# Optimization experiments

Measured on AMD Instinct MI355X. Metric: run time of the kernel, lower is better.

The kernel has to match this reference:

```python
import jax, jax.numpy as jnp
import numpy as np

NUM_HEADS = 16
D_MODEL = 1024
ROPE_THETA = 10000.0


def rope_cos_sin(H, W, head_dim, theta):
    # SAM2/SAM3 axial RoPE: first half of complex dims encode x, second half y.
    n = H * W
    t = jnp.arange(n)
    tx = (t % W).astype(jnp.float32)
    ty = (t // W).astype(jnp.float32)
    # freqs: 1 / theta^(arange(0, dim, 4)[:dim//4] / dim)
    exps = jnp.arange(0, head_dim, 4)[: head_dim // 4].astype(jnp.float32) / head_dim
    freqs = 1.0 / (theta ** exps)  # (head_dim//4,)
    ang = jnp.concatenate([tx[:, None] * freqs, ty[:, None] * freqs], axis=-1)  # (N, head_dim//2)
    return jnp.cos(ang), jnp.sin(ang)


def apply_rope(x, cos, sin):
    # x: (B, nh, N, D); pairs of features treated as complex numbers
    B, nh, N, D = x.shape
    xr = x.reshape(B, nh, N, D // 2, 2)
    xe, xo = xr[..., 0], xr[..., 1]
    oe = xe * cos - xo * sin
    oo = xe * sin + xo * cos
    return jnp.stack([oe, oo], axis=-1).reshape(B, nh, N, D)


def setup_inputs() -> dict:
    key = jax.random.key(0)
    ks = jax.random.split(key, 12)
    C = D_MODEL
    s = 1.0 / np.sqrt(C)
    inp = {
        "q": jax.random.normal(ks[0], (2, 2048, C), dtype=jnp.float32),
        "k": jax.random.normal(ks[1], (2, 2112, C), dtype=jnp.float32),
        "v": jax.random.normal(ks[2], (2, 2112, C), dtype=jnp.float32),
        "Wq": jax.random.normal(ks[3], (C, C), dtype=jnp.float32) * s,
        "bq": jax.random.normal(ks[4], (C,), dtype=jnp.float32) * s,
        "Wk": jax.random.normal(ks[5], (C, C), dtype=jnp.float32) * s,
        "bk": jax.random.normal(ks[6], (C,), dtype=jnp.float32) * s,
        "Wv": jax.random.normal(ks[7], (C, C), dtype=jnp.float32) * s,
        "bv": jax.random.normal(ks[8], (C,), dtype=jnp.float32) * s,
        "Wo": jax.random.normal(ks[9], (C, C), dtype=jnp.float32) * s,
        "bo": jax.random.normal(ks[10], (C,), dtype=jnp.float32) * s,
        "q_h": 32,
        "q_w": 64,
        "num_final_k_to_exclude": 64,
    }
    return inp


def reference(q, k, v, Wq, bq, Wk, bk, Wv, bv, Wo, bo, q_h, q_w, num_final_k_to_exclude):
    B, Nq, C = q.shape
    Nk = k.shape[1]
    nh = NUM_HEADS
    d = C // nh
    # QKV projections -> (B, nh, N, d)
    qh = (q @ Wq + bq).reshape(B, Nq, nh, d).transpose(0, 2, 1, 3)
    kh = (k @ Wk + bk).reshape(B, Nk, nh, d).transpose(0, 2, 1, 3)
    vh = (v @ Wv + bv).reshape(B, Nk, nh, d).transpose(0, 2, 1, 3)
    # RoPE on q and on first num_k_keep keys (exclude trailing pointer tokens)
    n_keep = Nk - num_final_k_to_exclude  # == q_h * q_w == Nq here
    cos, sin = rope_cos_sin(q_h, q_w, d, ROPE_THETA)
    qh = apply_rope(qh, cos, sin)
    k_rot = apply_rope(kh[:, :, :n_keep], cos, sin)
    kh = jnp.concatenate([k_rot, kh[:, :, n_keep:]], axis=2)
    # scaled dot-product attention
    scale = 1.0 / np.sqrt(d)
    scores = jnp.einsum("bhqd,bhkd->bhqk", qh, kh) * scale
    probs = jax.nn.softmax(scores, axis=-1)
    attn = jnp.einsum("bhqk,bhkd->bhqd", probs, vh)
    out = attn.transpose(0, 2, 1, 3).reshape(B, Nq, C)
    return out @ Wo + bo
```

## Files before the change

### kernel.cpp

```cpp
#include <hip/hip_runtime.h>

#define B_ 2
#define NQ 2048
#define NK 2112
#define CD 1024
#define NH 16
#define HD 64

typedef unsigned short u16;
typedef unsigned int u32;
typedef __attribute__((ext_vector_type(8))) __bf16 bf16x8;
typedef __attribute__((ext_vector_type(4))) float f32x4;

#define GPTR(p) ((const __attribute__((address_space(1))) void*)(p))
#define LPTR(p) ((__attribute__((address_space(3))) void*)(p))
#define GLL16(g, l) __builtin_amdgcn_global_load_lds(GPTR(g), LPTR(l), 16, 0, 0)

__device__ __forceinline__ u16 f2bf(float f) {
  u32 u = __float_as_uint(f);
  u32 r = u + 0x7fffu + ((u >> 16) & 1u);
  return (u16)(r >> 16);
}
__device__ __forceinline__ float bf2f(u16 h) { return __uint_as_float(((u32)h) << 16); }

#define SC 0.18033688011112042f
#define NEGL2T 0.8304820237f
#define FSTEP 0.5623413252f

__global__ void prep_kernel(const float* __restrict__ q, const float* __restrict__ k,
                            const float* __restrict__ v, u16* __restrict__ qb,
                            u16* __restrict__ kb, u16* __restrict__ vb,
                            const float* __restrict__ W0, const float* __restrict__ W1,
                            const float* __restrict__ W2, const float* __restrict__ W3,
                            u16* __restrict__ T0, u16* __restrict__ T1,
                            u16* __restrict__ T2, u16* __restrict__ T3) {
  __shared__ u16 tile[32][33];
  int y = blockIdx.y;
  int t = threadIdx.x;
  if (y < 3) {
    const float* src = (y == 0) ? q : (y == 1) ? k : v;
    u16* dst = (y == 0) ? qb : (y == 1) ? kb : vb;
    int n4 = (y == 0) ? (B_ * NQ * CD / 4) : (B_ * NK * CD / 4);
    int i = blockIdx.x * 256 + t;
    if (i >= n4) return;
    float4 vv = ((const float4*)src)[i];
    ushort4 o;
    o.x = f2bf(vv.x); o.y = f2bf(vv.y); o.z = f2bf(vv.z); o.w = f2bf(vv.w);
    ((ushort4*)dst)[i] = o;
  } else {
    int x = blockIdx.x;
    if (x >= 4096) return;
    int which = x >> 10, xy = x & 1023;
    const float* src = (which == 0) ? W0 : (which == 1) ? W1 : (which == 2) ? W2 : W3;
    u16* dst = (which == 0) ? T0 : (which == 1) ? T1 : (which == 2) ? T2 : T3;
    int r0 = (xy >> 5) * 32, c0 = (xy & 31) * 32;
    int row = t >> 3, c4 = (t & 7) * 4;
    float4 vv = *(const float4*)&src[(r0 + row) * 1024 + c0 + c4];
    tile[row][c4 + 0] = f2bf(vv.x);
    tile[row][c4 + 1] = f2bf(vv.y);
    tile[row][c4 + 2] = f2bf(vv.z);
    tile[row][c4 + 3] = f2bf(vv.w);
    __syncthreads();
    ushort4 o;
    o.x = tile[c4 + 0][row];
    o.y = tile[c4 + 1][row];
    o.z = tile[c4 + 2][row];
    o.w = tile[c4 + 3][row];
    *(ushort4*)&dst[(c0 + row) * 1024 + r0 + c4] = o;
  }
}

__global__ __launch_bounds__(256, 2) void gemm_qkv(
    const u16* __restrict__ qb, const u16* __restrict__ kb, const u16* __restrict__ vb,
    const u16* __restrict__ wqt, const u16* __restrict__ wkt, const u16* __restrict__ wvt,
    const float* __restrict__ bq, const float* __restrict__ bk, const float* __restrict__ bv,
    u16* __restrict__ Qh, u16* __restrict__ Kh, u16* __restrict__ Vt) {
  __shared__ u16 As[128 * 32];
  __shared__ u16 Bs[128 * 32];
  const int z = blockIdx.z;
  if (z == 0 && blockIdx.y >= 32) return;
  const u16* A = (z == 0) ? qb : (z == 1) ? kb : vb;
  const u16* Bt = (z == 0) ? wqt : (z == 1) ? wkt : wvt;
  const float* bias = (z == 0) ? bq : (z == 1) ? bk : bv;
  const int BR = (z == 0) ? NQ : NK;

  const int t = threadIdx.x;
  const int lane = t & 63, w = t >> 6;
  const int lc = lane & 15, lq = lane >> 4;
  const int m0 = blockIdx.y * 128, n0 = blockIdx.x * 128;
  const int wm = (w >> 1) * 64, wn = (w & 1) * 64;
  f32x4 acc[4][4] = {};
  const u16* ga = A + (m0 + (t >> 2)) * 1024 + (t & 3) * 8;
  const u16* gb = Bt + (n0 + (t >> 2)) * 1024 + (t & 3) * 8;
  char* lA = (char*)As + w * 1024;
  char* lB = (char*)Bs + w * 1024;
  const bool swap = (z < 2);
  for (int k0 = 0; k0 < 1024; k0 += 32) {
    if (k0) __syncthreads();
    GLL16(ga + k0, lA);
    GLL16(ga + 64 * 1024 + k0, lA + 4096);
    GLL16(gb + k0, lB);
    GLL16(gb + 64 * 1024 + k0, lB + 4096);
    __syncthreads();
    bf16x8 af[4], bf[4];
#pragma unroll
    for (int i = 0; i < 4; ++i) {
      af[i] = *(const bf16x8*)&As[(wm + i * 16 + lc) * 32 + lq * 8];
      bf[i] = *(const bf16x8*)&Bs[(wn + i * 16 + lc) * 32 + lq * 8];
    }
    if (swap) {
#pragma unroll
      for (int mi = 0; mi < 4; ++mi)
#pragma unroll
        for (int ni = 0; ni < 4; ++ni)
          acc[mi][ni] = __builtin_amdgcn_mfma_f32_16x16x32_bf16(bf[ni], af[mi], acc[mi][ni], 0, 0, 0);
    } else {
#pragma unroll
      for (int mi = 0; mi < 4; ++mi)
#pragma unroll
        for (int ni = 0; ni < 4; ++ni)
          acc[mi][ni] = __builtin_amdgcn_mfma_f32_16x16x32_bf16(af[mi], bf[ni], acc[mi][ni], 0, 0, 0);
    }
  }

  if (swap) {
    u16* Out = (z == 0) ? Qh : Kh;
    const bool isQ = (z == 0);
#pragma unroll
    for (int ni = 0; ni < 4; ++ni) {
      int cb = n0 + wn + ni * 16 + lq * 4;
      float4 bv4 = *(const float4*)&bias[cb];
      int jj = (ni * 8 + lq * 2) & 15;
      bool jl = ni < 2;
      float f0 = exp2f((float)jj * -NEGL2T);
      float f1 = f0 * FSTEP;
#pragma unroll
      for (int mi = 0; mi < 4; ++mi) {
        int row = m0 + wm + mi * 16 + lc;
        int bb = row >= BR ? 1 : 0;
        int tok = row - bb * BR;
        float v0 = acc[mi][ni][0] + bv4.x;
        float v1 = acc[mi][ni][1] + bv4.y;
        float v2 = acc[mi][ni][2] + bv4.z;
        float v3 = acc[mi][ni][3] + bv4.w;
        uint2 pk;
        if (isQ || tok < 2048) {
          float pos = jl ? (float)(tok & 63) : (float)(tok >> 6);
          float s0, c0, s1, c1;
          __sincosf(pos * f0, &s0, &c0);
          __sincosf(pos * f1, &s1, &c1);
          float o0 = v0 * c0 - v1 * s0, o1 = v0 * s0 + v1 * c0;
          float o2 = v2 * c1 - v3 * s1, o3 = v2 * s1 + v3 * c1;
          if (isQ) { o0 *= SC; o1 *= SC; o2 *= SC; o3 *= SC; }
          pk.x = (u32)f2bf(o0) | ((u32)f2bf(o1) << 16);
          pk.y = (u32)f2bf(o2) | ((u32)f2bf(o3) << 16);
        } else {
          pk.x = (u32)f2bf(v0) | ((u32)f2bf(v1) << 16);
          pk.y = (u32)f2bf(v2) | ((u32)f2bf(v3) << 16);
        }
        *(uint2*)&Out[row * 1024 + cb] = pk;
      }
    }
  } else {
#pragma unroll
    for (int ni = 0; ni < 4; ++ni) {
      int col = n0 + wn + ni * 16 + lc;
      float bv = bias[col];
      int hh = col >> 6, dd = col & 63;
#pragma unroll
      for (int mi = 0; mi < 4; ++mi) {
        int row0 = m0 + wm + mi * 16 + lq * 4;
        int bb = row0 >= NK ? 1 : 0;
        int tok0 = row0 - bb * NK;
        float v0 = acc[mi][ni][0] + bv;
        float v1 = acc[mi][ni][1] + bv;
        float v2 = acc[mi][ni][2] + bv;
        float v3 = acc[mi][ni][3] + bv;
        uint2 pk;
        pk.x = (u32)f2bf(v0) | ((u32)f2bf(v1) << 16);
        pk.y = (u32)f2bf(v2) | ((u32)f2bf(v3) << 16);
        *(uint2*)&Vt[((bb * NH + hh) * HD + dd) * NK + tok0] = pk;
      }
    }
  }
}

__global__ __launch_bounds__(256, 2) void gemm_o(const u16* __restrict__ A,
                                                 const u16* __restrict__ Bt,
                                                 const float* __restrict__ bias,
                                                 float* __restrict__ Cout) {
  __shared__ u16 As[128 * 32];
  __shared__ u16 Bs[64 * 32];
  const int t = threadIdx.x;
  const int lane = t & 63, w = t >> 6;
  const int lc = lane & 15, lq = lane >> 4;
  const int m0 = blockIdx.y * 128, n0 = blockIdx.x * 64;
  const int wm = (w >> 1) * 64, wn = (w & 1) * 32;
  f32x4 acc[4][2] = {};
  const u16* ga = A + (m0 + (t >> 2)) * 1024 + (t & 3) * 8;
  const u16* gb = Bt + (n0 + (t >> 2)) * 1024 + (t & 3) * 8;
  char* lA = (char*)As + w * 1024;
  char* lB = (char*)Bs + w * 1024;
  for (int k0 = 0; k0 < 1024; k0 += 32) {
    if (k0) __syncthreads();
    GLL16(ga + k0, lA);
    GLL16(ga + 64 * 1024 + k0, lA + 4096);
    GLL16(gb + k0, lB);
    __syncthreads();
    bf16x8 af[4], bf[2];
#pragma unroll
    for (int i = 0; i < 4; ++i)
      af[i] = *(const bf16x8*)&As[(wm + i * 16 + lc) * 32 + lq * 8];
#pragma unroll
    for (int i = 0; i < 2; ++i)
      bf[i] = *(const bf16x8*)&Bs[(wn + i * 16 + lc) * 32 + lq * 8];
#pragma unroll
    for (int mi = 0; mi < 4; ++mi)
#pragma unroll
      for (int ni = 0; ni < 2; ++ni)
        acc[mi][ni] = __builtin_amdgcn_mfma_f32_16x16x32_bf16(bf[ni], af[mi], acc[mi][ni], 0, 0, 0);
  }
#pragma unroll
  for (int ni = 0; ni < 2; ++ni) {
    int cb = n0 + wn + ni * 16 + lq * 4;
    float4 bv4 = *(const float4*)&bias[cb];
#pragma unroll
    for (int mi = 0; mi < 4; ++mi) {
      int row = m0 + wm + mi * 16 + lc;
      float4 o;
      o.x = acc[mi][ni][0] + bv4.x;
      o.y = acc[mi][ni][1] + bv4.y;
      o.z = acc[mi][ni][2] + bv4.z;
      o.w = acc[mi][ni][3] + bv4.w;
      *(float4*)&Cout[row * 1024 + cb] = o;
    }
  }
}

#define LSTR 72
__global__ __launch_bounds__(256, 2) void attn_kernel(const u16* __restrict__ Qh,
                                                      const u16* __restrict__ Kh,
                                                      const u16* __restrict__ Vt,
                                                      u16* __restrict__ AO) {
  __shared__ u16 QPs[128 * LSTR];
  __shared__ u16 Ks[64 * LSTR];
  __shared__ u16 Vs[64 * LSTR];
  const int t = threadIdx.x;
  const int lane = t & 63, w = t >> 6;
  const int lc = lane & 15, lq = lane >> 4;
  const int rr = lane >> 3, s = lane & 7;
  const int qt = blockIdx.x, h = blockIdx.y, b = blockIdx.z;

  {
    const u16* gq = Qh + (b * NQ + qt * 128 + w * 32 + rr) * CD + h * HD + s * 8;
    u16* lqp = &QPs[(w * 32 + rr) * LSTR + s * 8];
#pragma unroll
    for (int i = 0; i < 4; ++i)
      *(uint4*)(lqp + i * 8 * LSTR) = *(const uint4*)(gq + i * 8 * CD);
  }
  bf16x8 qf[2][2];
#pragma unroll
  for (int ni = 0; ni < 2; ++ni)
#pragma unroll
    for (int kk = 0; kk < 2; ++kk)
      qf[ni][kk] = *(const bf16x8*)&QPs[(w * 32 + ni * 16 + lc) * LSTR + kk * 32 + lq * 8];

  bf16x8 ones;
  {
    u32* op = (u32*)&ones;
    op[0] = op[1] = op[2] = op[3] = 0x3F803F80u;
  }

  const u16* gK = Kh + (b * NK + w * 16 + rr) * CD + h * HD + s * 8;
  const u16* gV = Vt + ((b * NH + h) * HD + w * 16 + rr) * NK + s * 8;
  uint4 kreg0, kreg1, vreg0, vreg1;
  kreg0 = *(const uint4*)(gK);
  kreg1 = *(const uint4*)(gK + 8 * CD);
  vreg0 = *(const uint4*)(gV);
  vreg1 = *(const uint4*)(gV + 8 * NK);

  f32x4 oacc[2][4] = {};
  f32x4 lacc[2] = {};

  for (int j0 = 0; j0 < NK; j0 += 64) {
    __syncthreads();
    *(uint4*)&Ks[(w * 16 + rr) * LSTR + s * 8] = kreg0;
    *(uint4*)&Ks[(w * 16 + 8 + rr) * LSTR + s * 8] = kreg1;
    *(uint4*)&Vs[(w * 16 + rr) * LSTR + s * 8] = vreg0;
    *(uint4*)&Vs[(w * 16 + 8 + rr) * LSTR + s * 8] = vreg1;
    __syncthreads();
    if (j0 + 64 < NK) {
      kreg0 = *(const uint4*)(gK + (j0 + 64) * CD);
      kreg1 = *(const uint4*)(gK + (j0 + 64) * CD + 8 * CD);
      vreg0 = *(const uint4*)(gV + j0 + 64);
      vreg1 = *(const uint4*)(gV + 8 * NK + j0 + 64);
    }

    f32x4 st[2][4] = {};
#pragma unroll
    for (int mi = 0; mi < 4; ++mi) {
      bf16x8 k0f = *(const bf16x8*)&Ks[(mi * 16 + lc) * LSTR + lq * 8];
      bf16x8 k1f = *(const bf16x8*)&Ks[(mi * 16 + lc) * LSTR + 32 + lq * 8];
#pragma unroll
      for (int ni = 0; ni < 2; ++ni) {
        st[ni][mi] = __builtin_amdgcn_mfma_f32_16x16x32_bf16(k0f, qf[ni][0], st[ni][mi], 0, 0, 0);
        st[ni][mi] = __builtin_amdgcn_mfma_f32_16x16x32_bf16(k1f, qf[ni][1], st[ni][mi], 0, 0, 0);
      }
    }
#pragma unroll
    for (int ni = 0; ni < 2; ++ni)
#pragma unroll
      for (int mi = 0; mi < 4; ++mi) {
        u32 e0 = __float_as_uint(__builtin_amdgcn_exp2f(st[ni][mi][0])) + 0x8000u;
        u32 e1 = __float_as_uint(__builtin_amdgcn_exp2f(st[ni][mi][1])) + 0x8000u;
        u32 e2 = __float_as_uint(__builtin_amdgcn_exp2f(st[ni][mi][2])) + 0x8000u;
        u32 e3 = __float_as_uint(__builtin_amdgcn_exp2f(st[ni][mi][3])) + 0x8000u;
        uint2 pk;
        pk.x = __builtin_amdgcn_perm(e1, e0, 0x07060302u);
        pk.y = __builtin_amdgcn_perm(e3, e2, 0x07060302u);
        *(uint2*)&QPs[(w * 32 + ni * 16 + lc) * LSTR + mi * 16 + lq * 4] = pk;
      }
#pragma unroll
    for (int kc = 0; kc < 2; ++kc) {
      bf16x8 pf[2], vf[4];
#pragma unroll
      for (int ni = 0; ni < 2; ++ni)
        pf[ni] = *(const bf16x8*)&QPs[(w * 32 + ni * 16 + lc) * LSTR + kc * 32 + lq * 8];
#pragma unroll
      for (int di = 0; di < 4; ++di)
        vf[di] = *(const bf16x8*)&Vs[(di * 16 + lc) * LSTR + kc * 32 + lq * 8];
#pragma unroll
      for (int ni = 0; ni < 2; ++ni) {
#pragma unroll
        for (int di = 0; di < 4; ++di)
          oacc[ni][di] = __builtin_amdgcn_mfma_f32_16x16x32_bf16(pf[ni], vf[di], oacc[ni][di], 0, 0, 0);
        lacc[ni] = __builtin_amdgcn_mfma_f32_16x16x32_bf16(pf[ni], ones, lacc[ni], 0, 0, 0);
      }
    }
  }
#pragma unroll
  for (int ni = 0; ni < 2; ++ni)
#pragma unroll
    for (int r = 0; r < 4; ++r) {
      float inv = 1.0f / lacc[ni][r];
#pragma unroll
      for (int di = 0; di < 4; ++di) {
        int row = qt * 128 + w * 32 + ni * 16 + lq * 4 + r;
        int col = h * HD + di * 16 + lc;
        AO[(b * NQ + row) * CD + col] = f2bf(oacc[ni][di][r] * inv);
      }
    }
}

extern "C" void kernel_launch(void* const* d_in, const int* in_sizes, int n_in,
                              void* d_out, int out_size, void* d_ws, size_t ws_size,
                              hipStream_t stream) {
  const float* q  = (const float*)d_in[0];
  const float* k  = (const float*)d_in[1];
  const float* v  = (const float*)d_in[2];
  const float* Wq = (const float*)d_in[3];
  const float* bq = (const float*)d_in[4];
  const float* Wk = (const float*)d_in[5];
  const float* bk = (const float*)d_in[6];
  const float* Wv = (const float*)d_in[7];
  const float* bv = (const float*)d_in[8];
  const float* Wo = (const float*)d_in[9];
  const float* bo = (const float*)d_in[10];

  char* ws = (char*)d_ws;
  size_t off = 0;
  auto alloc = [&](size_t bytes) {
    char* p = ws + off;
    off += (bytes + 255) & ~(size_t)255;
    return p;
  };
  u16* qb  = (u16*)alloc((size_t)B_ * NQ * CD * 2);
  u16* kb  = (u16*)alloc((size_t)B_ * NK * CD * 2);
  u16* vb  = (u16*)alloc((size_t)B_ * NK * CD * 2);
  u16* wqt = (u16*)alloc((size_t)CD * CD * 2);
  u16* wkt = (u16*)alloc((size_t)CD * CD * 2);
  u16* wvt = (u16*)alloc((size_t)CD * CD * 2);
  u16* wot = (u16*)alloc((size_t)CD * CD * 2);
  u16* Qh  = (u16*)alloc((size_t)B_ * NQ * CD * 2);
  u16* Kh  = (u16*)alloc((size_t)B_ * NK * CD * 2);
  u16* Vt  = (u16*)alloc((size_t)B_ * NK * CD * 2);
  u16* AO  = (u16*)alloc((size_t)B_ * NQ * CD * 2);

  prep_kernel<<<dim3(4224, 4), 256, 0, stream>>>(q, k, v, qb, kb, vb,
                                                 Wq, Wk, Wv, Wo, wqt, wkt, wvt, wot);
  gemm_qkv<<<dim3(8, 33, 3), 256, 0, stream>>>(qb, kb, vb, wqt, wkt, wvt, bq, bk, bv, Qh, Kh, Vt);
  attn_kernel<<<dim3(16, NH, B_), 256, 0, stream>>>(Qh, Kh, Vt, AO);
  gemm_o<<<dim3(16, 32), 256, 0, stream>>>(AO, wot, bo, (float*)d_out);
}
```

Baseline: 261.3 us.

## Fuse fp32-to-bf16 input conversion into QKV GEMM and double-buffer attention K/V

The separate pass that converts q/k/v activations to bf16 is removed. The QKV GEMM now reads fp32 activations directly, converts them in registers, stores them to LDS, and prefetches the next k-slice. This avoids writing and re-reading a bf16 copy of the activations, at the cost of double the activation read bandwidth per tile and register-staged loads in place of direct global-to-LDS loads. The attention kernel gets double-buffered K/V shared tiles, which cuts one barrier per iteration, and the GEMM launch bound is raised to 3 blocks per CU.

```diff
diff --git a/kernel.cpp b/kernel.cpp
--- a/kernel.cpp
+++ b/kernel.cpp
@@ -21,57 +21,43 @@
   u32 r = u + 0x7fffu + ((u >> 16) & 1u);
   return (u16)(r >> 16);
 }
-__device__ __forceinline__ float bf2f(u16 h) { return __uint_as_float(((u32)h) << 16); }
+__device__ __forceinline__ u32 pack2bf(float x, float y) {
+  u32 a = __float_as_uint(x); a += 0x7fffu + ((a >> 16) & 1u);
+  u32 b = __float_as_uint(y); b += 0x7fffu + ((b >> 16) & 1u);
+  return __builtin_amdgcn_perm(b, a, 0x07060302u);
+}
 
 #define SC 0.18033688011112042f
 #define NEGL2T 0.8304820237f
 #define FSTEP 0.5623413252f
 
-__global__ void prep_kernel(const float* __restrict__ q, const float* __restrict__ k,
-                            const float* __restrict__ v, u16* __restrict__ qb,
-                            u16* __restrict__ kb, u16* __restrict__ vb,
-                            const float* __restrict__ W0, const float* __restrict__ W1,
+__global__ void prep_kernel(const float* __restrict__ W0, const float* __restrict__ W1,
                             const float* __restrict__ W2, const float* __restrict__ W3,
                             u16* __restrict__ T0, u16* __restrict__ T1,
                             u16* __restrict__ T2, u16* __restrict__ T3) {
   __shared__ u16 tile[32][33];
-  int y = blockIdx.y;
+  int which = blockIdx.y;
+  const float* src = (which == 0) ? W0 : (which == 1) ? W1 : (which == 2) ? W2 : W3;
+  u16* dst = (which == 0) ? T0 : (which == 1) ? T1 : (which == 2) ? T2 : T3;
   int t = threadIdx.x;
-  if (y < 3) {
-    const float* src = (y == 0) ? q : (y == 1) ? k : v;
-    u16* dst = (y == 0) ? qb : (y == 1) ? kb : vb;
-    int n4 = (y == 0) ? (B_ * NQ * CD / 4) : (B_ * NK * CD / 4);
-    int i = blockIdx.x * 256 + t;
-    if (i >= n4) return;
-    float4 vv = ((const float4*)src)[i];
-    ushort4 o;
-    o.x = f2bf(vv.x); o.y = f2bf(vv.y); o.z = f2bf(vv.z); o.w = f2bf(vv.w);
-    ((ushort4*)dst)[i] = o;
-  } else {
-    int x = blockIdx.x;
-    if (x >= 4096) return;
-    int which = x >> 10, xy = x & 1023;
-    const float* src = (which == 0) ? W0 : (which == 1) ? W1 : (which == 2) ? W2 : W3;
-    u16* dst = (which == 0) ? T0 : (which == 1) ? T1 : (which == 2) ? T2 : T3;
-    int r0 = (xy >> 5) * 32, c0 = (xy & 31) * 32;
-    int row = t >> 3, c4 = (t & 7) * 4;
-    float4 vv = *(const float4*)&src[(r0 + row) * 1024 + c0 + c4];
-    tile[row][c4 + 0] = f2bf(vv.x);
-    tile[row][c4 + 1] = f2bf(vv.y);
-    tile[row][c4 + 2] = f2bf(vv.z);
-    tile[row][c4 + 3] = f2bf(vv.w);
-    __syncthreads();
-    ushort4 o;
-    o.x = tile[c4 + 0][row];
-    o.y = tile[c4 + 1][row];
-    o.z = tile[c4 + 2][row];
-    o.w = tile[c4 + 3][row];
-    *(ushort4*)&dst[(c0 + row) * 1024 + r0 + c4] = o;
-  }
-}
-
-__global__ __launch_bounds__(256, 2) void gemm_qkv(
-    const u16* __restrict__ qb, const u16* __restrict__ kb, const u16* __restrict__ vb,
+  int r0 = (blockIdx.x >> 5) * 32, c0 = (blockIdx.x & 31) * 32;
+  int row = t >> 3, c4 = (t & 7) * 4;
+  float4 vv = *(const float4*)&src[(r0 + row) * 1024 + c0 + c4];
+  tile[row][c4 + 0] = f2bf(vv.x);
+  tile[row][c4 + 1] = f2bf(vv.y);
+  tile[row][c4 + 2] = f2bf(vv.z);
+  tile[row][c4 + 3] = f2bf(vv.w);
+  __syncthreads();
+  ushort4 o;
+  o.x = tile[c4 + 0][row];
+  o.y = tile[c4 + 1][row];
+  o.z = tile[c4 + 2][row];
+  o.w = tile[c4 + 3][row];
+  *(ushort4*)&dst[(c0 + row) * 1024 + r0 + c4] = o;
+}
+
+__global__ __launch_bounds__(256, 3) void gemm_qkv(
+    const float* __restrict__ qf32, const float* __restrict__ kf32, const float* __restrict__ vf32,
     const u16* __restrict__ wqt, const u16* __restrict__ wkt, const u16* __restrict__ wvt,
     const float* __restrict__ bq, const float* __restrict__ bk, const float* __restrict__ bv,
     u16* __restrict__ Qh, u16* __restrict__ Kh, u16* __restrict__ Vt) {
@@ -79,7 +65,7 @@
   __shared__ u16 Bs[128 * 32];
   const int z = blockIdx.z;
   if (z == 0 && blockIdx.y >= 32) return;
-  const u16* A = (z == 0) ? qb : (z == 1) ? kb : vb;
+  const float* A = (z == 0) ? qf32 : (z == 1) ? kf32 : vf32;
   const u16* Bt = (z == 0) ? wqt : (z == 1) ? wkt : wvt;
   const float* bias = (z == 0) ? bq : (z == 1) ? bk : bv;
   const int BR = (z == 0) ? NQ : NK;
@@ -90,17 +76,36 @@
   const int m0 = blockIdx.y * 128, n0 = blockIdx.x * 128;
   const int wm = (w >> 1) * 64, wn = (w & 1) * 64;
   f32x4 acc[4][4] = {};
-  const u16* ga = A + (m0 + (t >> 2)) * 1024 + (t & 3) * 8;
+  const float* ga = A + (m0 + (t >> 2)) * 1024 + (t & 3) * 8;
   const u16* gb = Bt + (n0 + (t >> 2)) * 1024 + (t & 3) * 8;
-  char* lA = (char*)As + w * 1024;
+  u16* sa = &As[(t >> 2) * 32 + (t & 3) * 8];
   char* lB = (char*)Bs + w * 1024;
   const bool swap = (z < 2);
+
+  float4 a0 = *(const float4*)(ga);
+  float4 a1 = *(const float4*)(ga + 4);
+  float4 a2 = *(const float4*)(ga + 64 * 1024);
+  float4 a3 = *(const float4*)(ga + 64 * 1024 + 4);
+
   for (int k0 = 0; k0 < 1024; k0 += 32) {
     if (k0) __syncthreads();
-    GLL16(ga + k0, lA);
-    GLL16(ga + 64 * 1024 + k0, lA + 4096);
+    {
+      uint4 p0, p1;
+      p0.x = pack2bf(a0.x, a0.y); p0.y = pack2bf(a0.z, a0.w);
+      p0.z = pack2bf(a1.x, a1.y); p0.w = pack2bf(a1.z, a1.w);
+      p1.x = pack2bf(a2.x, a2.y); p1.y = pack2bf(a2.z, a2.w);
+      p1.z = pack2bf(a3.x, a3.y); p1.w = pack2bf(a3.z, a3.w);
+      *(uint4*)sa = p0;
+      *(uint4*)(sa + 64 * 32) = p1;
+    }
     GLL16(gb + k0, lB);
     GLL16(gb + 64 * 1024 + k0, lB + 4096);
+    if (k0 + 32 < 1024) {
+      a0 = *(const float4*)(ga + k0 + 32);
+      a1 = *(const float4*)(ga + k0 + 36);
+      a2 = *(const float4*)(ga + 64 * 1024 + k0 + 32);
+      a3 = *(const float4*)(ga + 64 * 1024 + k0 + 36);
+    }
     __syncthreads();
     bf16x8 af[4], bf[4];
 #pragma unroll
@@ -172,13 +177,9 @@
         int row0 = m0 + wm + mi * 16 + lq * 4;
         int bb = row0 >= NK ? 1 : 0;
         int tok0 = row0 - bb * NK;
-        float v0 = acc[mi][ni][0] + bv;
-        float v1 = acc[mi][ni][1] + bv;
-        float v2 = acc[mi][ni][2] + bv;
-        float v3 = acc[mi][ni][3] + bv;
         uint2 pk;
-        pk.x = (u32)f2bf(v0) | ((u32)f2bf(v1) << 16);
-        pk.y = (u32)f2bf(v2) | ((u32)f2bf(v3) << 16);
+        pk.x = pack2bf(acc[mi][ni][0] + bv, acc[mi][ni][1] + bv);
+        pk.y = pack2bf(acc[mi][ni][2] + bv, acc[mi][ni][3] + bv);
         *(uint2*)&Vt[((bb * NH + hh) * HD + dd) * NK + tok0] = pk;
       }
     }
@@ -243,8 +244,8 @@
                                                       const u16* __restrict__ Vt,
                                                       u16* __restrict__ AO) {
   __shared__ u16 QPs[128 * LSTR];
-  __shared__ u16 Ks[64 * LSTR];
-  __shared__ u16 Vs[64 * LSTR];
+  __shared__ u16 Ks[2 * 64 * LSTR];
+  __shared__ u16 Vs[2 * 64 * LSTR];
   const int t = threadIdx.x;
   const int lane = t & 63, w = t >> 6;
   const int lc = lane & 15, lq = lane >> 4;
@@ -273,34 +274,36 @@
 
   const u16* gK = Kh + (b * NK + w * 16 + rr) * CD + h * HD + s * 8;
   const u16* gV = Vt + ((b * NH + h) * HD + w * 16 + rr) * NK + s * 8;
-  uint4 kreg0, kreg1, vreg0, vreg1;
-  kreg0 = *(const uint4*)(gK);
-  kreg1 = *(const uint4*)(gK + 8 * CD);
-  vreg0 = *(const uint4*)(gV);
-  vreg1 = *(const uint4*)(gV + 8 * NK);
+  const int sk0 = (w * 16 + rr) * LSTR + s * 8;
+  const int sk1 = (w * 16 + 8 + rr) * LSTR + s * 8;
+
+  uint4 kreg0 = *(const uint4*)(gK);
+  uint4 kreg1 = *(const uint4*)(gK + 8 * CD);
+  uint4 vreg0 = *(const uint4*)(gV);
+  uint4 vreg1 = *(const uint4*)(gV + 8 * NK);
+  *(uint4*)&Ks[sk0] = kreg0;
+  *(uint4*)&Ks[sk1] = kreg1;
+  *(uint4*)&Vs[sk0] = vreg0;
+  *(uint4*)&Vs[sk1] = vreg1;
+  kreg0 = *(const uint4*)(gK + 64 * CD);
+  kreg1 = *(const uint4*)(gK + 64 * CD + 8 * CD);
+  vreg0 = *(const uint4*)(gV + 64);
+  vreg1 = *(const uint4*)(gV + 8 * NK + 64);
+  __syncthreads();
 
   f32x4 oacc[2][4] = {};
   f32x4 lacc[2] = {};
+  int p = 0;
 
   for (int j0 = 0; j0 < NK; j0 += 64) {
-    __syncthreads();
-    *(uint4*)&Ks[(w * 16 + rr) * LSTR + s * 8] = kreg0;
-    *(uint4*)&Ks[(w * 16 + 8 + rr) * LSTR + s * 8] = kreg1;
-    *(uint4*)&Vs[(w * 16 + rr) * LSTR + s * 8] = vreg0;
-    *(uint4*)&Vs[(w * 16 + 8 + rr) * LSTR + s * 8] = vreg1;
-    __syncthreads();
-    if (j0 + 64 < NK) {
-      kreg0 = *(const uint4*)(gK + (j0 + 64) * CD);
-      kreg1 = *(const uint4*)(gK + (j0 + 64) * CD + 8 * CD);
-      vreg0 = *(const uint4*)(gV + j0 + 64);
-      vreg1 = *(const uint4*)(gV + 8 * NK + j0 + 64);
-    }
+    const u16* Kc = &Ks[p * 64 * LSTR];
+    const u16* Vc = &Vs[p * 64 * LSTR];
 
     f32x4 st[2][4] = {};
 #pragma unroll
     for (int mi = 0; mi < 4; ++mi) {
-      bf16x8 k0f = *(const bf16x8*)&Ks[(mi * 16 + lc) * LSTR + lq * 8];
-      bf16x8 k1f = *(const bf16x8*)&Ks[(mi * 16 + lc) * LSTR + 32 + lq * 8];
+      bf16x8 k0f = *(const bf16x8*)&Kc[(mi * 16 + lc) * LSTR + lq * 8];
+      bf16x8 k1f = *(const bf16x8*)&Kc[(mi * 16 + lc) * LSTR + 32 + lq * 8];
 #pragma unroll
       for (int ni = 0; ni < 2; ++ni) {
         st[ni][mi] = __builtin_amdgcn_mfma_f32_16x16x32_bf16(k0f, qf[ni][0], st[ni][mi], 0, 0, 0);
@@ -311,13 +314,13 @@
     for (int ni = 0; ni < 2; ++ni)
 #pragma unroll
       for (int mi = 0; mi < 4; ++mi) {
-        u32 e0 = __float_as_uint(__builtin_amdgcn_exp2f(st[ni][mi][0])) + 0x8000u;
-        u32 e1 = __float_as_uint(__builtin_amdgcn_exp2f(st[ni][mi][1])) + 0x8000u;
-        u32 e2 = __float_as_uint(__builtin_amdgcn_exp2f(st[ni][mi][2])) + 0x8000u;
-        u32 e3 = __float_as_uint(__builtin_amdgcn_exp2f(st[ni][mi][3])) + 0x8000u;
+        u32 e0 = __float_as_uint(__builtin_amdgcn_exp2f(st[ni][mi][0]));
+        u32 e1 = __float_as_uint(__builtin_amdgcn_exp2f(st[ni][mi][1]));
+        u32 e2 = __float_as_uint(__builtin_amdgcn_exp2f(st[ni][mi][2]));
+        u32 e3 = __float_as_uint(__builtin_amdgcn_exp2f(st[ni][mi][3]));
         uint2 pk;
-        pk.x = __builtin_amdgcn_perm(e1, e0, 0x07060302u);
-        pk.y = __builtin_amdgcn_perm(e3, e2, 0x07060302u);
+        pk.x = __builtin_amdgcn_perm(e1 + 0x8000u, e0 + 0x8000u, 0x07060302u);
+        pk.y = __builtin_amdgcn_perm(e3 + 0x8000u, e2 + 0x8000u, 0x07060302u);
         *(uint2*)&QPs[(w * 32 + ni * 16 + lc) * LSTR + mi * 16 + lq * 4] = pk;
       }
 #pragma unroll
@@ -328,7 +331,7 @@
         pf[ni] = *(const bf16x8*)&QPs[(w * 32 + ni * 16 + lc) * LSTR + kc * 32 + lq * 8];
 #pragma unroll
       for (int di = 0; di < 4; ++di)
-        vf[di] = *(const bf16x8*)&Vs[(di * 16 + lc) * LSTR + kc * 32 + lq * 8];
+        vf[di] = *(const bf16x8*)&Vs[p * 64 * LSTR + (di * 16 + lc) * LSTR + kc * 32 + lq * 8];
 #pragma unroll
       for (int ni = 0; ni < 2; ++ni) {
 #pragma unroll
@@ -337,6 +340,24 @@
         lacc[ni] = __builtin_amdgcn_mfma_f32_16x16x32_bf16(pf[ni], ones, lacc[ni], 0, 0, 0);
       }
     }
+    (void)Vc;
+
+    if (j0 + 64 < NK) {
+      u16* Kn = &Ks[(p ^ 1) * 64 * LSTR];
+      u16* Vn = &Vs[(p ^ 1) * 64 * LSTR];
+      *(uint4*)&Kn[sk0] = kreg0;
+      *(uint4*)&Kn[sk1] = kreg1;
+      *(uint4*)&Vn[sk0] = vreg0;
+      *(uint4*)&Vn[sk1] = vreg1;
+      if (j0 + 128 < NK) {
+        kreg0 = *(const uint4*)(gK + (j0 + 128) * CD);
+        kreg1 = *(const uint4*)(gK + (j0 + 128) * CD + 8 * CD);
+        vreg0 = *(const uint4*)(gV + j0 + 128);
+        vreg1 = *(const uint4*)(gV + 8 * NK + j0 + 128);
+      }
+    }
+    __syncthreads();
+    p ^= 1;
   }
 #pragma unroll
   for (int ni = 0; ni < 2; ++ni)
@@ -374,9 +395,6 @@
     off += (bytes + 255) & ~(size_t)255;
     return p;
   };
-  u16* qb  = (u16*)alloc((size_t)B_ * NQ * CD * 2);
-  u16* kb  = (u16*)alloc((size_t)B_ * NK * CD * 2);
-  u16* vb  = (u16*)alloc((size_t)B_ * NK * CD * 2);
   u16* wqt = (u16*)alloc((size_t)CD * CD * 2);
   u16* wkt = (u16*)alloc((size_t)CD * CD * 2);
   u16* wvt = (u16*)alloc((size_t)CD * CD * 2);
@@ -386,9 +404,8 @@
   u16* Vt  = (u16*)alloc((size_t)B_ * NK * CD * 2);
   u16* AO  = (u16*)alloc((size_t)B_ * NQ * CD * 2);
 
-  prep_kernel<<<dim3(4224, 4), 256, 0, stream>>>(q, k, v, qb, kb, vb,
-                                                 Wq, Wk, Wv, Wo, wqt, wkt, wvt, wot);
-  gemm_qkv<<<dim3(8, 33, 3), 256, 0, stream>>>(qb, kb, vb, wqt, wkt, wvt, bq, bk, bv, Qh, Kh, Vt);
+  prep_kernel<<<dim3(1024, 4), 256, 0, stream>>>(Wq, Wk, Wv, Wo, wqt, wkt, wvt, wot);
+  gemm_qkv<<<dim3(8, 33, 3), 256, 0, stream>>>(q, k, v, wqt, wkt, wvt, bq, bk, bv, Qh, Kh, Vt);
   attn_kernel<<<dim3(16, NH, B_), 256, 0, stream>>>(Qh, Kh, Vt, AO);
   gemm_o<<<dim3(16, 32), 256, 0, stream>>>(AO, wot, bo, (float*)d_out);
 }
```

After: 457.0 us. 1.75x slower.
